# Optimization experiments

Hardware: AMD Instinct MI355X
Metric: run time of the kernel (lower is better)

## Reference

```python
import jax, jax.numpy as jnp
import numpy as np

N = 100000
E = 1600000
IN_C, HID_C, OUT_C = 128, 128, 64


def setup_inputs() -> dict:
    key = jax.random.key(0)
    ks = jax.random.split(key, 8)
    x = jax.random.normal(ks[0], (N, IN_C), dtype=jnp.float32)
    edge_index = jax.random.randint(ks[1], (2, E), 0, N, dtype=jnp.int64)
    # Glorot-ish init for the 3 GCNConv linear weights + zero biases (PyG default)
    def glorot(k, fan_in, fan_out):
        s = jnp.sqrt(6.0 / (fan_in + fan_out))
        return jax.random.uniform(k, (fan_in, fan_out), jnp.float32, -s, s)
    return {
        "x": x,
        "edge_index": edge_index,
        "W1": glorot(ks[2], IN_C, HID_C), "b1": jnp.zeros((HID_C,), jnp.float32),
        "W2": glorot(ks[3], HID_C, HID_C), "b2": jnp.zeros((HID_C,), jnp.float32),
        "W3": glorot(ks[4], HID_C, OUT_C), "b3": jnp.zeros((OUT_C,), jnp.float32),
    }


def _gcn_norm(edge_index, num_nodes):
    # add self loops, compute D^-1/2 (A+I) D^-1/2 edge coefficients (PyG gcn_norm)
    loop = jnp.arange(num_nodes, dtype=edge_index.dtype)
    src = jnp.concatenate([edge_index[0], loop])  # [E+N]
    dst = jnp.concatenate([edge_index[1], loop])
    w = jnp.ones_like(src, dtype=jnp.float32)
    deg = jax.ops.segment_sum(w, dst, num_segments=num_nodes)
    dinv = jnp.where(deg > 0, jax.lax.rsqrt(deg), 0.0)
    norm = dinv[src] * dinv[dst]  # [E+N]
    return src, dst, norm


def _gcn_layer(x, src, dst, norm, W, b, num_nodes):
    h = x @ W                                   # [N, out]
    msg = h[src] * norm[:, None]                # gather + scale, [E+N, out]
    agg = jax.ops.segment_sum(msg, dst, num_segments=num_nodes)  # scatter-add
    return agg + b


def reference(x, edge_index, W1, b1, W2, b2, W3, b3):
    src, dst, norm = _gcn_norm(edge_index, N)
    h = jax.nn.relu(_gcn_layer(x, src, dst, norm, W1, b1, N))
    h = jax.nn.relu(_gcn_layer(h, src, dst, norm, W2, b2, N))
    h = _gcn_layer(h, src, dst, norm, W3, b3, N)
    return jax.nn.log_softmax(h, axis=-1)  # [N, OUT_C]
```

## Files before the change

kernel.cpp:

```cpp
#include <hip/hip_runtime.h>
#include <hip/hip_bf16.h>


constexpr int N_NODES = 100000;
constexpr int E_EDGES = 1600000;
constexpr int NB = (N_NODES + 127) / 128;
constexpr int BCAP = 2560;
constexpr int CHUNK = 8192;
constexpr int NCHUNK = (E_EDGES + CHUNK - 1) / CHUNK;

typedef short bf16x8 __attribute__((ext_vector_type(8)));
typedef float f32x4 __attribute__((ext_vector_type(4)));

__device__ __forceinline__ unsigned short f2bf(float f) {
    unsigned u = __float_as_uint(f);
    unsigned r = (u + 0x7fff + ((u >> 16) & 1)) >> 16;
    return (unsigned short)r;
}
__device__ __forceinline__ float bf_lo(unsigned u) { return __uint_as_float(u << 16); }
__device__ __forceinline__ float bf_hi(unsigned u) { return __uint_as_float(u & 0xffff0000u); }
__device__ __forceinline__ unsigned pack2bf(float lo, float hi) {
    return (unsigned)f2bf(lo) | ((unsigned)f2bf(hi) << 16);
}

__device__ __forceinline__ int get_idx(const void* ei, int use64, long long pos) {
    if (use64) return (int)((const long long*)ei)[pos];
    return ((const int*)ei)[pos];
}

__global__ void prep_wt_kernel(const float* __restrict__ W1, const float* __restrict__ W2,
                               const float* __restrict__ W3,
                               unsigned short* __restrict__ WT1,
                               unsigned short* __restrict__ WT2,
                               unsigned short* __restrict__ WT3,
                               const int* __restrict__ ei32, int* __restrict__ flag) {
    const int b = blockIdx.x;
    if (b == 3) {
        if (threadIdx.x == 0) {
            int ok64 = 1;
#pragma unroll
            for (int i = 1; i < 64; i += 2) ok64 &= (ei32[i] == 0);
            *flag = ok64;
        }
        return;
    }
    const float* W = (b == 0) ? W1 : (b == 1) ? W2 : W3;
    unsigned short* WT = (b == 0) ? WT1 : (b == 1) ? WT2 : WT3;
    const int COUT = (b == 2) ? 64 : 128;
    for (int i = threadIdx.x; i < COUT * 128; i += blockDim.x) {
        int c = i >> 7;
        int k = i & 127;
        WT[c * 128 + k] = f2bf(W[k * COUT + c]);
    }
}

__global__ __launch_bounds__(256) void scatter_direct(
    const void* __restrict__ ei, const int* __restrict__ flag,
    int* __restrict__ cursorPad, unsigned* __restrict__ pairs) {
    __shared__ int h[NB];
    __shared__ int base[NB];
    __shared__ unsigned dstb[CHUNK];
    const int t = threadIdx.x;
    const int use64 = *flag;
    const int e0 = blockIdx.x * CHUNK;
    const int e1 = min(E_EDGES, e0 + CHUNK);

    for (int i = t; i < NB; i += 256) h[i] = 0;
    __syncthreads();
    for (int e = e0 + t; e < e1; e += 256) {
        unsigned d = (unsigned)get_idx(ei, use64, (long long)E_EDGES + e);
        dstb[e - e0] = d;
        atomicAdd(&h[d >> 7], 1);
    }
    __syncthreads();
    for (int i = t; i < NB; i += 256) {
        int c = h[i];
        if (c) base[i] = atomicAdd(&cursorPad[i * 16], c);
        h[i] = 0;
    }
    __syncthreads();
    for (int e = e0 + t; e < e1; e += 256) {
        unsigned s = (unsigned)get_idx(ei, use64, e);
        unsigned d = dstb[e - e0];
        int b = d >> 7;
        int r = base[b] + atomicAdd(&h[b], 1);
        if (r < BCAP) pairs[(unsigned)b * BCAP + r] = (s << 7) | (d & 127u);
    }
}

__global__ __launch_bounds__(256) void fine_sort_kernel(
    const unsigned* __restrict__ pairs, const int* __restrict__ cursorPad,
    int* __restrict__ csr, int* __restrict__ rowptr, int* __restrict__ deg,
    float* __restrict__ dinv) {
    __shared__ int h[128];
    __shared__ int rp[128];
    __shared__ int sc[128];
    const int t = threadIdx.x;
    const int b = blockIdx.x;
    const int base = b * BCAP;
    const int cnt = min(cursorPad[b * 16], BCAP);

    if (t < 128) h[t] = 0;
    __syncthreads();
    for (int i = t; i < cnt; i += 256) {
        unsigned p = pairs[base + i];
        atomicAdd(&h[p & 127u], 1);
    }
    __syncthreads();
    int v = (t < 128) ? h[t] : 0;
    if (t < 128) sc[t] = v;
    __syncthreads();
    int incl = v;
    for (int off = 1; off < 128; off <<= 1) {
        int add = (t >= off && t < 128) ? sc[t - off] : 0;
        __syncthreads();
        if (t < 128) {
            incl += add;
            sc[t] = incl;
        }
        __syncthreads();
    }
    if (t < 128) {
        rp[t] = incl - v;
        int node = b * 128 + t;
        if (node < N_NODES) {
            rowptr[node] = base + incl - v;
            deg[node] = v;
            dinv[node] = rsqrtf((float)(v + 1));
        }
        h[t] = 0;
    }
    __syncthreads();
    for (int i = t; i < cnt; i += 256) {
        unsigned p = pairs[base + i];
        int l = (int)(p & 127u);
        int r = atomicAdd(&h[l], 1);
        csr[base + rp[l] + r] = (int)(p >> 7);
    }
}

__global__ __launch_bounds__(256) void deg_hist_kernel(const int* __restrict__ deg,
                                                       int* __restrict__ degHistPad) {
    __shared__ int lh[64];
    const int t = threadIdx.x;
    if (t < 64) lh[t] = 0;
    __syncthreads();
    int n = blockIdx.x * 256 + t;
    if (n < N_NODES) atomicAdd(&lh[min(deg[n], 63)], 1);
    __syncthreads();
    if (t < 64 && lh[t]) atomicAdd(&degHistPad[t * 16], lh[t]);
}

__global__ void scan_bins_kernel(int* __restrict__ degHistPad) {
    const int t = threadIdx.x;
    int v = degHistPad[t * 16];
    int incl = v;
#pragma unroll
    for (int off = 1; off < 64; off <<= 1) {
        int o = __shfl_up(incl, off);
        if (t >= off) incl += o;
    }
    degHistPad[t * 16] = incl - v;
}

__global__ __launch_bounds__(256) void build_perm_kernel(
    const int* __restrict__ deg, const int* __restrict__ rowptr,
    const float* __restrict__ dinv, int* __restrict__ degCursorPad,
    int4* __restrict__ nodeinfo) {
    __shared__ int lh[64];
    __shared__ int lbase[64];
    const int t = threadIdx.x;
    if (t < 64) lh[t] = 0;
    __syncthreads();
    const int n = blockIdx.x * 256 + t;
    int bin = 0, dv = 0;
    if (n < N_NODES) {
        dv = deg[n];
        bin = min(dv, 63);
        atomicAdd(&lh[bin], 1);
    }
    __syncthreads();
    if (t < 64) {
        int c = lh[t];
        lbase[t] = c ? atomicAdd(&degCursorPad[t * 16], c) : 0;
        lh[t] = 0;
    }
    __syncthreads();
    if (n < N_NODES) {
        int r = atomicAdd(&lh[bin], 1);
        nodeinfo[lbase[bin] + r] = make_int4(rowptr[n], dv, __float_as_int(dinv[n]), n);
    }
}

template <int COUT>
__global__ __launch_bounds__(256) void gemm_mfma_f32(const float* __restrict__ X,
                                                     const unsigned short* __restrict__ WT,
                                                     const float* __restrict__ dinv,
                                                     unsigned short* __restrict__ H) {
    constexpr int NT = COUT / 16;
    __shared__ short Albs[64 * 128];
    __shared__ short Wlds[COUT * 128];

    const int t = threadIdx.x;
    const int row0 = blockIdx.x * 64;

    for (int i = t; i < COUT * 16; i += 256) {
        int n = i >> 4, k8 = i & 15;
        bf16x8 v = *(const bf16x8*)&WT[n * 128 + k8 * 8];
        *(bf16x8*)&Wlds[(k8 * COUT + n) * 8] = v;
    }
    for (int i = t; i < 1024; i += 256) {
        int m = i >> 4, k8 = i & 15;
        int gr = min(row0 + m, N_NODES - 1);
        const float* p = &X[(size_t)gr * 128 + k8 * 8];
        float4 f0 = *(const float4*)p;
        float4 f1 = *(const float4*)(p + 4);
        bf16x8 v;
        v[0] = (short)f2bf(f0.x); v[1] = (short)f2bf(f0.y);
        v[2] = (short)f2bf(f0.z); v[3] = (short)f2bf(f0.w);
        v[4] = (short)f2bf(f1.x); v[5] = (short)f2bf(f1.y);
        v[6] = (short)f2bf(f1.z); v[7] = (short)f2bf(f1.w);
        int u = ((m >> 4) * 16 + (k8 >> 2) * 4 + (k8 & 3)) * 16 + (m & 15);
        *(bf16x8*)&Albs[u * 8] = v;
    }
    __syncthreads();

    const int lane = t & 63;
    const int wv = t >> 6;
    const int l15 = lane & 15;
    const int quad = lane >> 4;

    f32x4 acc[NT];
#pragma unroll
    for (int ct = 0; ct < NT; ct++) acc[ct] = (f32x4){0.f, 0.f, 0.f, 0.f};

#pragma unroll
    for (int kcg = 0; kcg < 4; kcg++) {
        bf16x8 a = *(const bf16x8*)&Albs[((wv * 16 + kcg * 4 + quad) * 16 + l15) * 8];
#pragma unroll
        for (int ct = 0; ct < NT; ct++) {
            bf16x8 b = *(const bf16x8*)&Wlds[((kcg * 4 + quad) * COUT + ct * 16 + l15) * 8];
            acc[ct] = __builtin_amdgcn_mfma_f32_16x16x32_bf16(a, b, acc[ct], 0, 0, 0);
        }
    }

    const int m0 = row0 + wv * 16;
#pragma unroll
    for (int r = 0; r < 4; r++) {
        int m = m0 + quad * 4 + r;
        if (m < N_NODES) {
            float dv = dinv[m];
#pragma unroll
            for (int ct = 0; ct < NT; ct++)
                H[(size_t)m * COUT + ct * 16 + l15] = f2bf(acc[ct][r] * dv);
        } else if (m == N_NODES) {
#pragma unroll
            for (int ct = 0; ct < NT; ct++)
                H[(size_t)m * COUT + ct * 16 + l15] = 0;
        }
    }
}

template <int COUT>
__global__ __launch_bounds__(256) void gemm_mfma_bf16(const unsigned short* __restrict__ X,
                                                      const unsigned short* __restrict__ WT,
                                                      const float* __restrict__ dinv,
                                                      unsigned short* __restrict__ H) {
    constexpr int NT = COUT / 16;
    __shared__ short Albs[64 * 128];
    __shared__ short Wlds[COUT * 128];

    const int t = threadIdx.x;
    const int row0 = blockIdx.x * 64;

    for (int i = t; i < COUT * 16; i += 256) {
        int n = i >> 4, k8 = i & 15;
        bf16x8 v = *(const bf16x8*)&WT[n * 128 + k8 * 8];
        *(bf16x8*)&Wlds[(k8 * COUT + n) * 8] = v;
    }
    for (int i = t; i < 1024; i += 256) {
        int m = i >> 4, k8 = i & 15;
        int gr = min(row0 + m, N_NODES - 1);
        bf16x8 v = *(const bf16x8*)&X[(size_t)gr * 128 + k8 * 8];
        int u = ((m >> 4) * 16 + (k8 >> 2) * 4 + (k8 & 3)) * 16 + (m & 15);
        *(bf16x8*)&Albs[u * 8] = v;
    }
    __syncthreads();

    const int lane = t & 63;
    const int wv = t >> 6;
    const int l15 = lane & 15;
    const int quad = lane >> 4;

    f32x4 acc[NT];
#pragma unroll
    for (int ct = 0; ct < NT; ct++) acc[ct] = (f32x4){0.f, 0.f, 0.f, 0.f};

#pragma unroll
    for (int kcg = 0; kcg < 4; kcg++) {
        bf16x8 a = *(const bf16x8*)&Albs[((wv * 16 + kcg * 4 + quad) * 16 + l15) * 8];
#pragma unroll
        for (int ct = 0; ct < NT; ct++) {
            bf16x8 b = *(const bf16x8*)&Wlds[((kcg * 4 + quad) * COUT + ct * 16 + l15) * 8];
            acc[ct] = __builtin_amdgcn_mfma_f32_16x16x32_bf16(a, b, acc[ct], 0, 0, 0);
        }
    }

    const int m0 = row0 + wv * 16;
#pragma unroll
    for (int r = 0; r < 4; r++) {
        int m = m0 + quad * 4 + r;
        if (m < N_NODES) {
            float dv = dinv[m];
#pragma unroll
            for (int ct = 0; ct < NT; ct++)
                H[(size_t)m * COUT + ct * 16 + l15] = f2bf(acc[ct][r] * dv);
        } else if (m == N_NODES) {
#pragma unroll
            for (int ct = 0; ct < NT; ct++)
                H[(size_t)m * COUT + ct * 16 + l15] = 0;
        }
    }
}

__global__ __launch_bounds__(256) void aggregate128_pair(
    const unsigned short* __restrict__ Hb, const int4* __restrict__ nodeinfo,
    const int* __restrict__ csr, const float* __restrict__ bias,
    unsigned short* __restrict__ out) {
    const int lane = threadIdx.x & 63;
    const int wv = threadIdx.x >> 6;
    const int li = lane & 31;
    const int half = lane >> 5;
    const int gi = blockIdx.x * 8 + wv * 2 + half;
    const unsigned li8 = (unsigned)li * 8u;
    const char* Hc = (const char*)Hb;

    const int4 info = nodeinfo[gi];
    const int start = info.x;
    const int dc = info.y;
    const float dn = __int_as_float(info.z);
    const int n = info.w;

    uint2 s = *(const uint2*)(Hc + (size_t)n * 256u + li8);
    float a0 = bf_lo(s.x), a1 = bf_hi(s.x), a2 = bf_lo(s.y), a3 = bf_hi(s.y);

    const int dmax = max(dc, __shfl_xor(dc, 32));

    for (int eb = 0; eb < dmax; eb += 32) {
        int myidx = N_NODES;
        if (eb + li < dc) myidx = csr[start + eb + li];
        const int jmax = min(32, dmax - eb);
        int j = 0;
        for (; j + 8 <= jmax; j += 8) {
            int idx[8];
            uint2 u[8];
#pragma unroll
            for (int q = 0; q < 8; q++) idx[q] = __shfl(myidx, j + q, 32);
#pragma unroll
            for (int q = 0; q < 8; q++)
                u[q] = *(const uint2*)(Hc + (((unsigned)idx[q] << 8) + li8));
#pragma unroll
            for (int q = 0; q < 8; q++) {
                a0 += bf_lo(u[q].x); a1 += bf_hi(u[q].x);
                a2 += bf_lo(u[q].y); a3 += bf_hi(u[q].y);
            }
        }
        for (; j + 4 <= jmax; j += 4) {
            int idx[4];
            uint2 u[4];
#pragma unroll
            for (int q = 0; q < 4; q++) idx[q] = __shfl(myidx, j + q, 32);
#pragma unroll
            for (int q = 0; q < 4; q++)
                u[q] = *(const uint2*)(Hc + (((unsigned)idx[q] << 8) + li8));
#pragma unroll
            for (int q = 0; q < 4; q++) {
                a0 += bf_lo(u[q].x); a1 += bf_hi(u[q].x);
                a2 += bf_lo(u[q].y); a3 += bf_hi(u[q].y);
            }
        }
        for (; j < jmax; j++) {
            int i0 = __shfl(myidx, j, 32);
            uint2 u0 = *(const uint2*)(Hc + (((unsigned)i0 << 8) + li8));
            a0 += bf_lo(u0.x); a1 += bf_hi(u0.x);
            a2 += bf_lo(u0.y); a3 += bf_hi(u0.y);
        }
    }

    float4 bv = *(const float4*)((const char*)bias + li * 16);
    uint2 o;
    o.x = pack2bf(fmaxf(a0 * dn + bv.x, 0.f), fmaxf(a1 * dn + bv.y, 0.f));
    o.y = pack2bf(fmaxf(a2 * dn + bv.z, 0.f), fmaxf(a3 * dn + bv.w, 0.f));
    *(uint2*)((char*)out + (size_t)n * 256 + li * 8) = o;
}

__global__ __launch_bounds__(256) void aggregate64_lsm_pair(
    const unsigned short* __restrict__ Hb, const int4* __restrict__ nodeinfo,
    const int* __restrict__ csr, const float* __restrict__ bias,
    float* __restrict__ out) {
    const int lane = threadIdx.x & 63;
    const int wv = threadIdx.x >> 6;
    const int li = lane & 31;
    const int half = lane >> 5;
    const int gi = blockIdx.x * 8 + wv * 2 + half;
    const unsigned li4 = (unsigned)li * 4u;
    const char* Hc = (const char*)Hb;

    const int4 info = nodeinfo[gi];
    const int start = info.x;
    const int dc = info.y;
    const float dn = __int_as_float(info.z);
    const int n = info.w;

    unsigned s = *(const unsigned*)(Hc + (size_t)n * 128u + li4);
    float a0 = bf_lo(s), a1 = bf_hi(s);

    const int dmax = max(dc, __shfl_xor(dc, 32));

    for (int eb = 0; eb < dmax; eb += 32) {
        int myidx = N_NODES;
        if (eb + li < dc) myidx = csr[start + eb + li];
        const int jmax = min(32, dmax - eb);
        int j = 0;
        for (; j + 8 <= jmax; j += 8) {
            int idx[8];
            unsigned u[8];
#pragma unroll
            for (int q = 0; q < 8; q++) idx[q] = __shfl(myidx, j + q, 32);
#pragma unroll
            for (int q = 0; q < 8; q++)
                u[q] = *(const unsigned*)(Hc + (((unsigned)idx[q] << 7) + li4));
#pragma unroll
            for (int q = 0; q < 8; q++) { a0 += bf_lo(u[q]); a1 += bf_hi(u[q]); }
        }
        for (; j + 4 <= jmax; j += 4) {
            int idx[4];
            unsigned u[4];
#pragma unroll
            for (int q = 0; q < 4; q++) idx[q] = __shfl(myidx, j + q, 32);
#pragma unroll
            for (int q = 0; q < 4; q++)
                u[q] = *(const unsigned*)(Hc + (((unsigned)idx[q] << 7) + li4));
#pragma unroll
            for (int q = 0; q < 4; q++) { a0 += bf_lo(u[q]); a1 += bf_hi(u[q]); }
        }
        for (; j < jmax; j++) {
            int i0 = __shfl(myidx, j, 32);
            unsigned u0 = *(const unsigned*)(Hc + (((unsigned)i0 << 7) + li4));
            a0 += bf_lo(u0); a1 += bf_hi(u0);
        }
    }

    float2 bv = *(const float2*)((const char*)bias + li * 8);
    float v0 = a0 * dn + bv.x;
    float v1 = a1 * dn + bv.y;

    float m = fmaxf(v0, v1);
#pragma unroll
    for (int off = 16; off; off >>= 1) m = fmaxf(m, __shfl_xor(m, off));
    float e = expf(v0 - m) + expf(v1 - m);
#pragma unroll
    for (int off = 16; off; off >>= 1) e += __shfl_xor(e, off);
    float lse = m + logf(e);
    float2 o = make_float2(v0 - lse, v1 - lse);
    *(float2*)((char*)out + (size_t)n * 256 + li * 8) = o;
}

extern "C" void kernel_launch(void* const* d_in, const int* in_sizes, int n_in,
                              void* d_out, int out_size, void* d_ws, size_t ws_size,
                              hipStream_t stream) {
    const float* x = (const float*)d_in[0];
    const void* ei = d_in[1];
    const float* W1 = (const float*)d_in[2];
    const float* b1 = (const float*)d_in[3];
    const float* W2 = (const float*)d_in[4];
    const float* b2 = (const float*)d_in[5];
    const float* W3 = (const float*)d_in[6];
    const float* b3 = (const float*)d_in[7];
    float* out = (float*)d_out;

    char* w = (char*)d_ws;
    size_t off = 0;
    auto take = [&](size_t bytes) {
        char* p = w + off;
        off = (off + bytes + 255) & ~(size_t)255;
        return p;
    };
    int* flag = (int*)take(4);
    int* cursorPad = (int*)take((size_t)NB * 64 + 64 * 64);
    int* degHistPad = cursorPad + NB * 16;
    int* deg = (int*)take((size_t)N_NODES * 4);
    int* rowptr = (int*)take((size_t)N_NODES * 4);
    float* dinv = (float*)take((size_t)N_NODES * 4);
    int* csr = (int*)take((size_t)NB * BCAP * 4);
    int4* nodeinfo = (int4*)take((size_t)N_NODES * 16);
    unsigned short* WT1 = (unsigned short*)take(128 * 128 * 2);
    unsigned short* WT2 = (unsigned short*)take(128 * 128 * 2);
    unsigned short* WT3 = (unsigned short*)take(64 * 128 * 2);
    unsigned short* A = (unsigned short*)take((size_t)(N_NODES + 1) * 128 * 2);
    unsigned short* B = (unsigned short*)take((size_t)N_NODES * 128 * 2);
    unsigned* pairs = (unsigned*)A;

    hipMemsetAsync(cursorPad, 0, (size_t)NB * 64 + 64 * 64, stream);
    prep_wt_kernel<<<4, 256, 0, stream>>>(W1, W2, W3, WT1, WT2, WT3, (const int*)ei, flag);
    scatter_direct<<<NCHUNK, 256, 0, stream>>>(ei, flag, cursorPad, pairs);
    fine_sort_kernel<<<NB, 256, 0, stream>>>(pairs, cursorPad, csr, rowptr, deg, dinv);
    deg_hist_kernel<<<(N_NODES + 255) / 256, 256, 0, stream>>>(deg, degHistPad);
    scan_bins_kernel<<<1, 64, 0, stream>>>(degHistPad);
    build_perm_kernel<<<(N_NODES + 255) / 256, 256, 0, stream>>>(deg, rowptr, dinv,
                                                                 degHistPad, nodeinfo);

    const int gg = (N_NODES + 63) / 64 + 1;
    const int gagg = N_NODES / 8;

    gemm_mfma_f32<128><<<gg, 256, 0, stream>>>(x, WT1, dinv, A);
    aggregate128_pair<<<gagg, 256, 0, stream>>>(A, nodeinfo, csr, b1, B);
    gemm_mfma_bf16<128><<<gg, 256, 0, stream>>>(B, WT2, dinv, A);
    aggregate128_pair<<<gagg, 256, 0, stream>>>(A, nodeinfo, csr, b2, B);
    gemm_mfma_bf16<64><<<gg, 256, 0, stream>>>(B, WT3, dinv, A);
    aggregate64_lsm_pair<<<gagg, 256, 0, stream>>>(A, nodeinfo, csr, b3, out);
}
```

Before: 383.8 us.

## Drop degree-sorted node permutation, unroll gathers by 16, halve scatter chunk

Removes the three kernels that histogrammed degrees and built a degree-sorted node permutation, so the aggregation kernels now index nodes directly and read rowptr, deg and dinv separately. This cuts three launches plus one preprocessing pass, at the cost of worse load balance between the paired half-waves, because neighbouring nodes no longer have similar degrees. It also adds a 16-wide unrolled gather path to keep more loads in flight, which raises register pressure. The scatter chunk is halved to launch more blocks.

```diff
diff --git a/kernel.cpp b/kernel.cpp
--- a/kernel.cpp
+++ b/kernel.cpp
@@ -6,7 +6,7 @@
 constexpr int E_EDGES = 1600000;
 constexpr int NB = (N_NODES + 127) / 128;
 constexpr int BCAP = 2560;
-constexpr int CHUNK = 8192;
+constexpr int CHUNK = 4096;
 constexpr int NCHUNK = (E_EDGES + CHUNK - 1) / CHUNK;
 
 typedef short bf16x8 __attribute__((ext_vector_type(8)));
@@ -136,59 +136,6 @@
         int l = (int)(p & 127u);
         int r = atomicAdd(&h[l], 1);
         csr[base + rp[l] + r] = (int)(p >> 7);
-    }
-}
-
-__global__ __launch_bounds__(256) void deg_hist_kernel(const int* __restrict__ deg,
-                                                       int* __restrict__ degHistPad) {
-    __shared__ int lh[64];
-    const int t = threadIdx.x;
-    if (t < 64) lh[t] = 0;
-    __syncthreads();
-    int n = blockIdx.x * 256 + t;
-    if (n < N_NODES) atomicAdd(&lh[min(deg[n], 63)], 1);
-    __syncthreads();
-    if (t < 64 && lh[t]) atomicAdd(&degHistPad[t * 16], lh[t]);
-}
-
-__global__ void scan_bins_kernel(int* __restrict__ degHistPad) {
-    const int t = threadIdx.x;
-    int v = degHistPad[t * 16];
-    int incl = v;
-#pragma unroll
-    for (int off = 1; off < 64; off <<= 1) {
-        int o = __shfl_up(incl, off);
-        if (t >= off) incl += o;
-    }
-    degHistPad[t * 16] = incl - v;
-}
-
-__global__ __launch_bounds__(256) void build_perm_kernel(
-    const int* __restrict__ deg, const int* __restrict__ rowptr,
-    const float* __restrict__ dinv, int* __restrict__ degCursorPad,
-    int4* __restrict__ nodeinfo) {
-    __shared__ int lh[64];
-    __shared__ int lbase[64];
-    const int t = threadIdx.x;
-    if (t < 64) lh[t] = 0;
-    __syncthreads();
-    const int n = blockIdx.x * 256 + t;
-    int bin = 0, dv = 0;
-    if (n < N_NODES) {
-        dv = deg[n];
-        bin = min(dv, 63);
-        atomicAdd(&lh[bin], 1);
-    }
-    __syncthreads();
-    if (t < 64) {
-        int c = lh[t];
-        lbase[t] = c ? atomicAdd(&degCursorPad[t * 16], c) : 0;
-        lh[t] = 0;
-    }
-    __syncthreads();
-    if (n < N_NODES) {
-        int r = atomicAdd(&lh[bin], 1);
-        nodeinfo[lbase[bin] + r] = make_int4(rowptr[n], dv, __float_as_int(dinv[n]), n);
     }
 }
 
@@ -324,26 +271,23 @@
 }
 
 __global__ __launch_bounds__(256) void aggregate128_pair(
-    const unsigned short* __restrict__ Hb, const int4* __restrict__ nodeinfo,
-    const int* __restrict__ csr, const float* __restrict__ bias,
+    const unsigned short* __restrict__ Hb, const int* __restrict__ rowptr,
+    const int* __restrict__ deg, const int* __restrict__ csr,
+    const float* __restrict__ dinv, const float* __restrict__ bias,
     unsigned short* __restrict__ out) {
     const int lane = threadIdx.x & 63;
     const int wv = threadIdx.x >> 6;
     const int li = lane & 31;
     const int half = lane >> 5;
-    const int gi = blockIdx.x * 8 + wv * 2 + half;
+    const int n = blockIdx.x * 8 + wv * 2 + half;
     const unsigned li8 = (unsigned)li * 8u;
     const char* Hc = (const char*)Hb;
 
-    const int4 info = nodeinfo[gi];
-    const int start = info.x;
-    const int dc = info.y;
-    const float dn = __int_as_float(info.z);
-    const int n = info.w;
-
     uint2 s = *(const uint2*)(Hc + (size_t)n * 256u + li8);
     float a0 = bf_lo(s.x), a1 = bf_hi(s.x), a2 = bf_lo(s.y), a3 = bf_hi(s.y);
 
+    const int start = rowptr[n];
+    const int dc = deg[n];
     const int dmax = max(dc, __shfl_xor(dc, 32));
 
     for (int eb = 0; eb < dmax; eb += 32) {
@@ -351,6 +295,20 @@
         if (eb + li < dc) myidx = csr[start + eb + li];
         const int jmax = min(32, dmax - eb);
         int j = 0;
+        for (; j + 16 <= jmax; j += 16) {
+            int idx[16];
+            uint2 u[16];
+#pragma unroll
+            for (int q = 0; q < 16; q++) idx[q] = __shfl(myidx, j + q, 32);
+#pragma unroll
+            for (int q = 0; q < 16; q++)
+                u[q] = *(const uint2*)(Hc + (((unsigned)idx[q] << 8) + li8));
+#pragma unroll
+            for (int q = 0; q < 16; q++) {
+                a0 += bf_lo(u[q].x); a1 += bf_hi(u[q].x);
+                a2 += bf_lo(u[q].y); a3 += bf_hi(u[q].y);
+            }
+        }
         for (; j + 8 <= jmax; j += 8) {
             int idx[8];
             uint2 u[8];
@@ -387,6 +345,7 @@
         }
     }
 
+    const float dn = dinv[n];
     float4 bv = *(const float4*)((const char*)bias + li * 16);
     uint2 o;
     o.x = pack2bf(fmaxf(a0 * dn + bv.x, 0.f), fmaxf(a1 * dn + bv.y, 0.f));
@@ -395,26 +354,23 @@
 }
 
 __global__ __launch_bounds__(256) void aggregate64_lsm_pair(
-    const unsigned short* __restrict__ Hb, const int4* __restrict__ nodeinfo,
-    const int* __restrict__ csr, const float* __restrict__ bias,
+    const unsigned short* __restrict__ Hb, const int* __restrict__ rowptr,
+    const int* __restrict__ deg, const int* __restrict__ csr,
+    const float* __restrict__ dinv, const float* __restrict__ bias,
     float* __restrict__ out) {
     const int lane = threadIdx.x & 63;
     const int wv = threadIdx.x >> 6;
     const int li = lane & 31;
     const int half = lane >> 5;
-    const int gi = blockIdx.x * 8 + wv * 2 + half;
+    const int n = blockIdx.x * 8 + wv * 2 + half;
     const unsigned li4 = (unsigned)li * 4u;
     const char* Hc = (const char*)Hb;
 
-    const int4 info = nodeinfo[gi];
-    const int start = info.x;
-    const int dc = info.y;
-    const float dn = __int_as_float(info.z);
-    const int n = info.w;
-
     unsigned s = *(const unsigned*)(Hc + (size_t)n * 128u + li4);
     float a0 = bf_lo(s), a1 = bf_hi(s);
 
+    const int start = rowptr[n];
+    const int dc = deg[n];
     const int dmax = max(dc, __shfl_xor(dc, 32));
 
     for (int eb = 0; eb < dmax; eb += 32) {
@@ -422,6 +378,17 @@
         if (eb + li < dc) myidx = csr[start + eb + li];
         const int jmax = min(32, dmax - eb);
         int j = 0;
+        for (; j + 16 <= jmax; j += 16) {
+            int idx[16];
+            unsigned u[16];
+#pragma unroll
+            for (int q = 0; q < 16; q++) idx[q] = __shfl(myidx, j + q, 32);
+#pragma unroll
+            for (int q = 0; q < 16; q++)
+                u[q] = *(const unsigned*)(Hc + (((unsigned)idx[q] << 7) + li4));
+#pragma unroll
+            for (int q = 0; q < 16; q++) { a0 += bf_lo(u[q]); a1 += bf_hi(u[q]); }
+        }
         for (; j + 8 <= jmax; j += 8) {
             int idx[8];
             unsigned u[8];
@@ -451,6 +418,7 @@
         }
     }
 
+    const float dn = dinv[n];
     float2 bv = *(const float2*)((const char*)bias + li * 8);
     float v0 = a0 * dn + bv.x;
     float v1 = a1 * dn + bv.y;
@@ -487,13 +455,11 @@
         return p;
     };
     int* flag = (int*)take(4);
-    int* cursorPad = (int*)take((size_t)NB * 64 + 64 * 64);
-    int* degHistPad = cursorPad + NB * 16;
+    int* cursorPad = (int*)take((size_t)NB * 64);
     int* deg = (int*)take((size_t)N_NODES * 4);
     int* rowptr = (int*)take((size_t)N_NODES * 4);
     float* dinv = (float*)take((size_t)N_NODES * 4);
     int* csr = (int*)take((size_t)NB * BCAP * 4);
-    int4* nodeinfo = (int4*)take((size_t)N_NODES * 16);
     unsigned short* WT1 = (unsigned short*)take(128 * 128 * 2);
     unsigned short* WT2 = (unsigned short*)take(128 * 128 * 2);
     unsigned short* WT3 = (unsigned short*)take(64 * 128 * 2);
@@ -501,22 +467,18 @@
     unsigned short* B = (unsigned short*)take((size_t)N_NODES * 128 * 2);
     unsigned* pairs = (unsigned*)A;
 
-    hipMemsetAsync(cursorPad, 0, (size_t)NB * 64 + 64 * 64, stream);
+    hipMemsetAsync(cursorPad, 0, (size_t)NB * 64, stream);
     prep_wt_kernel<<<4, 256, 0, stream>>>(W1, W2, W3, WT1, WT2, WT3, (const int*)ei, flag);
     scatter_direct<<<NCHUNK, 256, 0, stream>>>(ei, flag, cursorPad, pairs);
     fine_sort_kernel<<<NB, 256, 0, stream>>>(pairs, cursorPad, csr, rowptr, deg, dinv);
-    deg_hist_kernel<<<(N_NODES + 255) / 256, 256, 0, stream>>>(deg, degHistPad);
-    scan_bins_kernel<<<1, 64, 0, stream>>>(degHistPad);
-    build_perm_kernel<<<(N_NODES + 255) / 256, 256, 0, stream>>>(deg, rowptr, dinv,
-                                                                 degHistPad, nodeinfo);
 
     const int gg = (N_NODES + 63) / 64 + 1;
     const int gagg = N_NODES / 8;
 
     gemm_mfma_f32<128><<<gg, 256, 0, stream>>>(x, WT1, dinv, A);
-    aggregate128_pair<<<gagg, 256, 0, stream>>>(A, nodeinfo, csr, b1, B);
+    aggregate128_pair<<<gagg, 256, 0, stream>>>(A, rowptr, deg, csr, dinv, b1, B);
     gemm_mfma_bf16<128><<<gg, 256, 0, stream>>>(B, WT2, dinv, A);
-    aggregate128_pair<<<gagg, 256, 0, stream>>>(A, nodeinfo, csr, b2, B);
+    aggregate128_pair<<<gagg, 256, 0, stream>>>(A, rowptr, deg, csr, dinv, b2, B);
     gemm_mfma_bf16<64><<<gg, 256, 0, stream>>>(B, WT3, dinv, A);
-    aggregate64_lsm_pair<<<gagg, 256, 0, stream>>>(A, nodeinfo, csr, b3, out);
-}
+    aggregate64_lsm_pair<<<gagg, 256, 0, stream>>>(A, rowptr, deg, csr, dinv, b3, out);
+}
```

New measurement: 366.4 us. 4.5% less time.
